# Optimization experiments

Measured on AMD Instinct MI355X. Metric: run time of the kernel, lower is better.

The kernel has to match this reference:

```python
import jax, jax.numpy as jnp
import numpy as np

B, N, EMB, H, DH = 1, 196, 256, 8, 32
HID = 4 * EMB
EPS = 1e-5
SCALE = 16.0  # emb_size ** 0.5 (torch code scales by emb_size, not head_dim)


def _ln(x, w, b):
    m = jnp.mean(x, axis=-1, keepdims=True)
    v = jnp.mean((x - m) ** 2, axis=-1, keepdims=True)
    return (x - m) * jax.lax.rsqrt(v + EPS) * w + b


def _qkv(x, W, bias):
    # rearrange 'b n (h d qkv) -> qkv b h n d'
    t = (x @ W + bias).reshape(B, N, H, DH, 3)
    t = jnp.transpose(t, (4, 0, 2, 1, 3))
    return t[0], t[1], t[2]


def _attn(q, k, v, Wp, bp):
    att = jax.nn.softmax(jnp.einsum('bhqd,bhkd->bhqk', q, k) / SCALE, axis=-1)
    o = jnp.einsum('bhqk,bhkd->bhqd', att, v)
    o = jnp.transpose(o, (0, 2, 1, 3)).reshape(B, N, EMB)  # b n (h d)
    return o @ Wp + bp


def _ff(x, W1, b1, W2, b2):
    return jax.nn.gelu(x @ W1 + b1, approximate=False) @ W2 + b2


def _recon(x):
    x = x.reshape(B, 14, 14, 16, 16)
    x = jnp.transpose(x, (0, 3, 4, 1, 2))
    return x.reshape(B, 1, 224, 224)


def setup_inputs() -> dict:
    key = jax.random.key(0)
    ks = jax.random.split(key, 16)
    rn = lambda k, shape: jax.random.normal(k, shape, jnp.float32) * 0.02
    d = {
        'vis_emb': jax.random.normal(ks[0], (B, N, EMB), jnp.float32),
        'ir_emb': jax.random.normal(ks[1], (B, N, EMB), jnp.float32),
        'ln1v_w': jnp.ones((EMB,), jnp.float32), 'ln1v_b': jnp.zeros((EMB,), jnp.float32),
        'ln1i_w': jnp.ones((EMB,), jnp.float32), 'ln1i_b': jnp.zeros((EMB,), jnp.float32),
        'ln2v_w': jnp.ones((EMB,), jnp.float32), 'ln2v_b': jnp.zeros((EMB,), jnp.float32),
        'ln2i_w': jnp.ones((EMB,), jnp.float32), 'ln2i_b': jnp.zeros((EMB,), jnp.float32),
        'Wqkv_v': rn(ks[2], (EMB, 3 * EMB)), 'bqkv_v': jnp.zeros((3 * EMB,), jnp.float32),
        'Wqkv_i': rn(ks[3], (EMB, 3 * EMB)), 'bqkv_i': jnp.zeros((3 * EMB,), jnp.float32),
        'Wp_v': rn(ks[4], (EMB, EMB)), 'bp_v': jnp.zeros((EMB,), jnp.float32),
        'Wp_i': rn(ks[5], (EMB, EMB)), 'bp_i': jnp.zeros((EMB,), jnp.float32),
        'W1v': rn(ks[6], (EMB, HID)), 'b1v': jnp.zeros((HID,), jnp.float32),
        'W2v': rn(ks[7], (HID, EMB)), 'b2v': jnp.zeros((EMB,), jnp.float32),
        'W1i': rn(ks[8], (EMB, HID)), 'b1i': jnp.zeros((HID,), jnp.float32),
        'W2i': rn(ks[9], (HID, EMB)), 'b2i': jnp.zeros((EMB,), jnp.float32),
    }
    return d


def reference(vis_emb, ir_emb, ln1v_w, ln1v_b, ln1i_w, ln1i_b, ln2v_w, ln2v_b,
              ln2i_w, ln2i_b, Wqkv_v, bqkv_v, Wqkv_i, bqkv_i, Wp_v, bp_v,
              Wp_i, bp_i, W1v, b1v, W2v, b2v, W1i, b1i, W2i, b2i):
    nv = _ln(vis_emb, ln1v_w, ln1v_b)
    ni = _ln(ir_emb, ln1i_w, ln1i_b)
    qv, kv_, vv = _qkv(vis_emb, Wqkv_v, bqkv_v)
    qi, ki, vi = _qkv(ir_emb, Wqkv_i, bqkv_i)
    cross_v2i = _attn(qv, ki, vi, Wp_v, bp_v)   # vis queries attend ir k/v
    cross_i2v = _attn(qi, kv_, vv, Wp_i, bp_i)  # ir queries attend vis k/v
    rv = nv + cross_v2i
    ri = ni + cross_i2v
    lv = _ln(rv, ln2v_w, ln2v_b)
    li = _ln(ri, ln2i_w, ln2i_b)
    ov = _ff(lv, W1v, b1v, W2v, b2v) + lv
    oi = _ff(li, W1i, b1i, W2i, b2i) + li
    return jnp.concatenate([_recon(oi), _recon(ov)], axis=1)  # (1,2,224,224)
```

## Files before the change

kernel.cpp:

```cpp
#include <hip/hip_runtime.h>
#include <math.h>

#define NT   196
#define EMB  256
#define NH   8
#define DH   32
#define HID  1024
#define EPSV 1e-5f


__global__ __launch_bounds__(256) void k1_qkv(
    const float* __restrict__ vis, const float* __restrict__ ir,
    const float* __restrict__ Wqkv_v, const float* __restrict__ bqkv_v,
    const float* __restrict__ Wqkv_i, const float* __restrict__ bqkv_i,
    float* __restrict__ Q, float* __restrict__ Kq, float* __restrict__ Vq)
{
    const int b = blockIdx.x;
    const int s = b / 147;
    const int rem = b % 147;
    const int mt = rem / 3;
    const int cg = rem % 3;
    const int n0 = mt * 4;
    const int t = threadIdx.x;

    const float* x    = (s == 0) ? vis    : ir;
    const float* W    = (s == 0) ? Wqkv_v : Wqkv_i;
    const float* bias = (s == 0) ? bqkv_v : bqkv_i;

    __shared__ float xsT[EMB * 4];
    __shared__ float pp[4 * 4 * 256];

    {
        int r = t >> 6, c4 = (t & 63) * 4;
        float4 xv = *(const float4*)&x[(n0 + r) * EMB + c4];
        xsT[(c4 + 0) * 4 + r] = xv.x;
        xsT[(c4 + 1) * 4 + r] = xv.y;
        xsT[(c4 + 2) * 4 + r] = xv.z;
        xsT[(c4 + 3) * 4 + r] = xv.w;
    }
    __syncthreads();

    const int cq = t & 63, ks = t >> 6;
    const int col0 = cg * 256 + cq * 4;
    const float* Wb = W + col0;
    float4 a0 = {0,0,0,0}, a1 = a0, a2 = a0, a3 = a0;
    #pragma unroll 8
    for (int kk = ks * 64; kk < ks * 64 + 64; kk++) {
        float4 w4 = *(const float4*)&Wb[kk * 768];
        float4 xr = *(const float4*)&xsT[kk * 4];
        a0.x = fmaf(xr.x, w4.x, a0.x); a0.y = fmaf(xr.x, w4.y, a0.y);
        a0.z = fmaf(xr.x, w4.z, a0.z); a0.w = fmaf(xr.x, w4.w, a0.w);
        a1.x = fmaf(xr.y, w4.x, a1.x); a1.y = fmaf(xr.y, w4.y, a1.y);
        a1.z = fmaf(xr.y, w4.z, a1.z); a1.w = fmaf(xr.y, w4.w, a1.w);
        a2.x = fmaf(xr.z, w4.x, a2.x); a2.y = fmaf(xr.z, w4.y, a2.y);
        a2.z = fmaf(xr.z, w4.z, a2.z); a2.w = fmaf(xr.z, w4.w, a2.w);
        a3.x = fmaf(xr.w, w4.x, a3.x); a3.y = fmaf(xr.w, w4.y, a3.y);
        a3.z = fmaf(xr.w, w4.z, a3.z); a3.w = fmaf(xr.w, w4.w, a3.w);
    }
    *(float4*)&pp[(ks * 4 + 0) * 256 + cq * 4] = a0;
    *(float4*)&pp[(ks * 4 + 1) * 256 + cq * 4] = a1;
    *(float4*)&pp[(ks * 4 + 2) * 256 + cq * 4] = a2;
    *(float4*)&pp[(ks * 4 + 3) * 256 + cq * 4] = a3;
    __syncthreads();

    const int col = cg * 256 + t;
    const int h = col / 96, rr = col % 96, d = rr / 3, q = rr % 3;
    float* dst = (q == 0) ? Q : (q == 1 ? Kq : Vq);
    const float bval = bias[col];
    #pragma unroll
    for (int r = 0; r < 4; r++) {
        float v = pp[(0 * 4 + r) * 256 + t] + pp[(1 * 4 + r) * 256 + t]
                + pp[(2 * 4 + r) * 256 + t] + pp[(3 * 4 + r) * 256 + t] + bval;
        dst[((s * NH + h) * NT + n0 + r) * DH + d] = v;
    }
}

__global__ __launch_bounds__(256) void k2_attn(
    const float* __restrict__ Q, const float* __restrict__ Kq,
    const float* __restrict__ Vq, float* __restrict__ AO)
{
    const int b  = blockIdx.x;
    const int s  = b / 112;
    const int rm = b % 112;
    const int h  = rm / 14;
    const int rt = rm % 14;
    const int t    = threadIdx.x;
    const int wv   = t >> 6;
    const int lane = t & 63;

    __shared__ float kl[NT * 33];
    __shared__ float vl[NT * 33];
    __shared__ float pb[4][NT];

    const float4* Ks4 = (const float4*)(Kq + ((1 - s) * NH + h) * NT * DH);
    const float4* Vs4 = (const float4*)(Vq + ((1 - s) * NH + h) * NT * DH);
    for (int idx = t; idx < NT * 8; idx += 256) {
        int j = idx >> 3, d4 = (idx & 7) * 4;
        float4 kv = Ks4[idx];
        kl[j * 33 + d4 + 0] = kv.x; kl[j * 33 + d4 + 1] = kv.y;
        kl[j * 33 + d4 + 2] = kv.z; kl[j * 33 + d4 + 3] = kv.w;
        float4 vv = Vs4[idx];
        vl[j * 33 + d4 + 0] = vv.x; vl[j * 33 + d4 + 1] = vv.y;
        vl[j * 33 + d4 + 2] = vv.z; vl[j * 33 + d4 + 3] = vv.w;
    }
    __syncthreads();

    const float* Qs = Q + ((s * NH + h) * NT) * DH;
    const bool v3 = (lane + 192) < NT;
    const int  j3 = v3 ? (lane + 192) : 0;

    for (int it = 0; it < 4; it++) {
        int lr = it * 4 + wv;
        bool act = lr < 14;
        int i = rt * 14 + lr;
        float inv_sum = 0.0f;
        if (act) {
            float qreg[DH];
            #pragma unroll
            for (int d = 0; d < DH; d++) qreg[d] = Qs[i * DH + d];
            float s0 = 0.f, s1 = 0.f, s2 = 0.f, s3 = 0.f;
            #pragma unroll
            for (int d = 0; d < DH; d++) {
                float qd = qreg[d];
                s0 = fmaf(qd, kl[(lane      ) * 33 + d], s0);
                s1 = fmaf(qd, kl[(lane +  64) * 33 + d], s1);
                s2 = fmaf(qd, kl[(lane + 128) * 33 + d], s2);
                s3 = fmaf(qd, kl[ j3          * 33 + d], s3);
            }
            const float sc = 1.0f / 16.0f;
            s0 *= sc; s1 *= sc; s2 *= sc; s3 *= sc;
            float m = fmaxf(fmaxf(s0, s1), v3 ? fmaxf(s2, s3) : s2);
            #pragma unroll
            for (int mk = 32; mk >= 1; mk >>= 1) m = fmaxf(m, __shfl_xor(m, mk));
            float p0 = expf(s0 - m), p1 = expf(s1 - m), p2 = expf(s2 - m);
            float p3 = v3 ? expf(s3 - m) : 0.0f;
            float ls = p0 + p1 + p2 + p3;
            #pragma unroll
            for (int mk = 32; mk >= 1; mk >>= 1) ls += __shfl_xor(ls, mk);
            inv_sum = 1.0f / ls;
            pb[wv][lane]       = p0;
            pb[wv][lane +  64] = p1;
            pb[wv][lane + 128] = p2;
            if (v3) pb[wv][lane + 192] = p3;
        }
        __syncthreads();
        if (act) {
            int d = lane & 31, half = lane >> 5;
            float o = 0.0f;
            int jb = half * 98;
            for (int jj = 0; jj < 98; jj++) {
                int j = jb + jj;
                o = fmaf(pb[wv][j], vl[j * 33 + d], o);
            }
            o += __shfl_xor(o, 32);
            if (lane < 32) AO[(s * NT + i) * EMB + h * DH + d] = o * inv_sum;
        }
        __syncthreads();
    }
}

__global__ __launch_bounds__(256) void k3_proj_ln2(
    const float* __restrict__ vis, const float* __restrict__ ir,
    const float* __restrict__ AO,
    const float* __restrict__ ln1v_w, const float* __restrict__ ln1v_b,
    const float* __restrict__ ln1i_w, const float* __restrict__ ln1i_b,
    const float* __restrict__ Wp_v, const float* __restrict__ bp_v,
    const float* __restrict__ Wp_i, const float* __restrict__ bp_i,
    const float* __restrict__ ln2v_w, const float* __restrict__ ln2v_b,
    const float* __restrict__ ln2i_w, const float* __restrict__ ln2i_b,
    float* __restrict__ LV)
{
    const int b = blockIdx.x;
    const int s = b / 49;
    const int n0 = (b % 49) * 4;
    const int t = threadIdx.x;

    const float* x   = (s == 0) ? vis    : ir;
    const float* W   = (s == 0) ? Wp_v   : Wp_i;
    const float* bp  = (s == 0) ? bp_v   : bp_i;
    const float* l1w = (s == 0) ? ln1v_w : ln1i_w;
    const float* l1b = (s == 0) ? ln1v_b : ln1i_b;
    const float* l2w = (s == 0) ? ln2v_w : ln2i_w;
    const float* l2b = (s == 0) ? ln2v_b : ln2i_b;

    __shared__ float aoT[EMB * 4];
    __shared__ float pp[4 * 4 * 256];
    __shared__ float nvb[4 * 256];
    __shared__ float rbuf[4 * 256];

    const int r = t >> 6, lane = t & 63, c4 = lane * 4;

    {
        float4 xv = *(const float4*)&x[(n0 + r) * EMB + c4];
        float sum = xv.x + xv.y + xv.z + xv.w;
        float sq  = xv.x*xv.x + xv.y*xv.y + xv.z*xv.z + xv.w*xv.w;
        #pragma unroll
        for (int mk = 32; mk >= 1; mk >>= 1) {
            sum += __shfl_xor(sum, mk);
            sq  += __shfl_xor(sq,  mk);
        }
        float mean = sum * (1.0f / EMB);
        float inv  = rsqrtf(sq * (1.0f / EMB) - mean * mean + EPSV);
        float4 wv4 = *(const float4*)&l1w[c4];
        float4 bv4 = *(const float4*)&l1b[c4];
        nvb[r * 256 + c4 + 0] = (xv.x - mean) * inv * wv4.x + bv4.x;
        nvb[r * 256 + c4 + 1] = (xv.y - mean) * inv * wv4.y + bv4.y;
        nvb[r * 256 + c4 + 2] = (xv.z - mean) * inv * wv4.z + bv4.z;
        nvb[r * 256 + c4 + 3] = (xv.w - mean) * inv * wv4.w + bv4.w;
        float4 av = *(const float4*)&AO[(s * NT + n0 + r) * EMB + c4];
        aoT[(c4 + 0) * 4 + r] = av.x;
        aoT[(c4 + 1) * 4 + r] = av.y;
        aoT[(c4 + 2) * 4 + r] = av.z;
        aoT[(c4 + 3) * 4 + r] = av.w;
    }
    __syncthreads();

    const int cq = t & 63, ks = t >> 6;
    const int col0 = cq * 4;
    const float* Wb = W + col0;
    float4 a0 = {0,0,0,0}, a1 = a0, a2 = a0, a3 = a0;
    #pragma unroll 8
    for (int kk = ks * 64; kk < ks * 64 + 64; kk++) {
        float4 w4 = *(const float4*)&Wb[kk * EMB];
        float4 xr = *(const float4*)&aoT[kk * 4];
        a0.x = fmaf(xr.x, w4.x, a0.x); a0.y = fmaf(xr.x, w4.y, a0.y);
        a0.z = fmaf(xr.x, w4.z, a0.z); a0.w = fmaf(xr.x, w4.w, a0.w);
        a1.x = fmaf(xr.y, w4.x, a1.x); a1.y = fmaf(xr.y, w4.y, a1.y);
        a1.z = fmaf(xr.y, w4.z, a1.z); a1.w = fmaf(xr.y, w4.w, a1.w);
        a2.x = fmaf(xr.z, w4.x, a2.x); a2.y = fmaf(xr.z, w4.y, a2.y);
        a2.z = fmaf(xr.z, w4.z, a2.z); a2.w = fmaf(xr.z, w4.w, a2.w);
        a3.x = fmaf(xr.w, w4.x, a3.x); a3.y = fmaf(xr.w, w4.y, a3.y);
        a3.z = fmaf(xr.w, w4.z, a3.z); a3.w = fmaf(xr.w, w4.w, a3.w);
    }
    *(float4*)&pp[(ks * 4 + 0) * 256 + cq * 4] = a0;
    *(float4*)&pp[(ks * 4 + 1) * 256 + cq * 4] = a1;
    *(float4*)&pp[(ks * 4 + 2) * 256 + cq * 4] = a2;
    *(float4*)&pp[(ks * 4 + 3) * 256 + cq * 4] = a3;
    __syncthreads();

    {
        const float bval = bp[t];
        #pragma unroll
        for (int r2 = 0; r2 < 4; r2++) {
            float v = pp[(0 * 4 + r2) * 256 + t] + pp[(1 * 4 + r2) * 256 + t]
                    + pp[(2 * 4 + r2) * 256 + t] + pp[(3 * 4 + r2) * 256 + t]
                    + bval + nvb[r2 * 256 + t];
            rbuf[r2 * 256 + t] = v;
        }
    }
    __syncthreads();

    {
        float4 rv = *(const float4*)&rbuf[r * 256 + c4];
        float sum = rv.x + rv.y + rv.z + rv.w;
        float sq  = rv.x*rv.x + rv.y*rv.y + rv.z*rv.z + rv.w*rv.w;
        #pragma unroll
        for (int mk = 32; mk >= 1; mk >>= 1) {
            sum += __shfl_xor(sum, mk);
            sq  += __shfl_xor(sq,  mk);
        }
        float mean = sum * (1.0f / EMB);
        float inv  = rsqrtf(sq * (1.0f / EMB) - mean * mean + EPSV);
        float4 wv4 = *(const float4*)&l2w[c4];
        float4 bv4 = *(const float4*)&l2b[c4];
        float4 o;
        o.x = (rv.x - mean) * inv * wv4.x + bv4.x;
        o.y = (rv.y - mean) * inv * wv4.y + bv4.y;
        o.z = (rv.z - mean) * inv * wv4.z + bv4.z;
        o.w = (rv.w - mean) * inv * wv4.w + bv4.w;
        *(float4*)&LV[(s * NT + n0 + r) * EMB + c4] = o;
    }
}

__global__ __launch_bounds__(256) void k4_ffn1(
    const float* __restrict__ LV,
    const float* __restrict__ W1v, const float* __restrict__ b1v,
    const float* __restrict__ W1i, const float* __restrict__ b1i,
    float* __restrict__ HH)
{
    const int b = blockIdx.x;
    const int s = b / 196;
    const int rem = b % 196;
    const int mt = rem / 4;
    const int cg = rem % 4;
    const int n0 = mt * 4;
    const int t = threadIdx.x;

    const float* W  = (s == 0) ? W1v : W1i;
    const float* bb = (s == 0) ? b1v : b1i;

    __shared__ float xsT[EMB * 4];
    __shared__ float pp[4 * 4 * 256];

    {
        int r = t >> 6, c4 = (t & 63) * 4;
        float4 xv = *(const float4*)&LV[(s * NT + n0 + r) * EMB + c4];
        xsT[(c4 + 0) * 4 + r] = xv.x;
        xsT[(c4 + 1) * 4 + r] = xv.y;
        xsT[(c4 + 2) * 4 + r] = xv.z;
        xsT[(c4 + 3) * 4 + r] = xv.w;
    }
    __syncthreads();

    const int cq = t & 63, ks = t >> 6;
    const int col0 = cg * 256 + cq * 4;
    const float* Wb = W + col0;
    float4 a0 = {0,0,0,0}, a1 = a0, a2 = a0, a3 = a0;
    #pragma unroll 8
    for (int kk = ks * 64; kk < ks * 64 + 64; kk++) {
        float4 w4 = *(const float4*)&Wb[kk * HID];
        float4 xr = *(const float4*)&xsT[kk * 4];
        a0.x = fmaf(xr.x, w4.x, a0.x); a0.y = fmaf(xr.x, w4.y, a0.y);
        a0.z = fmaf(xr.x, w4.z, a0.z); a0.w = fmaf(xr.x, w4.w, a0.w);
        a1.x = fmaf(xr.y, w4.x, a1.x); a1.y = fmaf(xr.y, w4.y, a1.y);
        a1.z = fmaf(xr.y, w4.z, a1.z); a1.w = fmaf(xr.y, w4.w, a1.w);
        a2.x = fmaf(xr.z, w4.x, a2.x); a2.y = fmaf(xr.z, w4.y, a2.y);
        a2.z = fmaf(xr.z, w4.z, a2.z); a2.w = fmaf(xr.z, w4.w, a2.w);
        a3.x = fmaf(xr.w, w4.x, a3.x); a3.y = fmaf(xr.w, w4.y, a3.y);
        a3.z = fmaf(xr.w, w4.z, a3.z); a3.w = fmaf(xr.w, w4.w, a3.w);
    }
    *(float4*)&pp[(ks * 4 + 0) * 256 + cq * 4] = a0;
    *(float4*)&pp[(ks * 4 + 1) * 256 + cq * 4] = a1;
    *(float4*)&pp[(ks * 4 + 2) * 256 + cq * 4] = a2;
    *(float4*)&pp[(ks * 4 + 3) * 256 + cq * 4] = a3;
    __syncthreads();

    const int col = cg * 256 + t;
    const float bval = bb[col];
    #pragma unroll
    for (int r = 0; r < 4; r++) {
        float v = pp[(0 * 4 + r) * 256 + t] + pp[(1 * 4 + r) * 256 + t]
                + pp[(2 * 4 + r) * 256 + t] + pp[(3 * 4 + r) * 256 + t] + bval;
        float g = 0.5f * v * (1.0f + erff(v * 0.7071067811865475f));
        HH[(s * NT + n0 + r) * HID + col] = g;
    }
}

__global__ __launch_bounds__(256) void k5_ffn2_out(
    const float* __restrict__ HH, const float* __restrict__ LV,
    const float* __restrict__ W2v, const float* __restrict__ b2v,
    const float* __restrict__ W2i, const float* __restrict__ b2i,
    float* __restrict__ out)
{
    const int b = blockIdx.x;
    const int s = b / 49;
    const int n0 = (b % 49) * 4;
    const int t = threadIdx.x;

    const float* W  = (s == 0) ? W2v : W2i;
    const float* bb = (s == 0) ? b2v : b2i;

    __shared__ float hhT[HID * 4];
    __shared__ float pp[4 * 4 * 256];

    {
        int r = t >> 6, lane = t & 63;
        #pragma unroll
        for (int rd = 0; rd < 4; rd++) {
            int c4 = rd * 256 + lane * 4;
            float4 hv = *(const float4*)&HH[(s * NT + n0 + r) * HID + c4];
            hhT[(c4 + 0) * 4 + r] = hv.x;
            hhT[(c4 + 1) * 4 + r] = hv.y;
            hhT[(c4 + 2) * 4 + r] = hv.z;
            hhT[(c4 + 3) * 4 + r] = hv.w;
        }
    }
    __syncthreads();

    const int cq = t & 63, ks = t >> 6;
    const int col0 = cq * 4;
    const float* Wb = W + col0;
    float4 a0 = {0,0,0,0}, a1 = a0, a2 = a0, a3 = a0;
    #pragma unroll 8
    for (int kk = ks * 256; kk < ks * 256 + 256; kk++) {
        float4 w4 = *(const float4*)&Wb[kk * EMB];
        float4 xr = *(const float4*)&hhT[kk * 4];
        a0.x = fmaf(xr.x, w4.x, a0.x); a0.y = fmaf(xr.x, w4.y, a0.y);
        a0.z = fmaf(xr.x, w4.z, a0.z); a0.w = fmaf(xr.x, w4.w, a0.w);
        a1.x = fmaf(xr.y, w4.x, a1.x); a1.y = fmaf(xr.y, w4.y, a1.y);
        a1.z = fmaf(xr.y, w4.z, a1.z); a1.w = fmaf(xr.y, w4.w, a1.w);
        a2.x = fmaf(xr.z, w4.x, a2.x); a2.y = fmaf(xr.z, w4.y, a2.y);
        a2.z = fmaf(xr.z, w4.z, a2.z); a2.w = fmaf(xr.z, w4.w, a2.w);
        a3.x = fmaf(xr.w, w4.x, a3.x); a3.y = fmaf(xr.w, w4.y, a3.y);
        a3.z = fmaf(xr.w, w4.z, a3.z); a3.w = fmaf(xr.w, w4.w, a3.w);
    }
    *(float4*)&pp[(ks * 4 + 0) * 256 + cq * 4] = a0;
    *(float4*)&pp[(ks * 4 + 1) * 256 + cq * 4] = a1;
    *(float4*)&pp[(ks * 4 + 2) * 256 + cq * 4] = a2;
    *(float4*)&pp[(ks * 4 + 3) * 256 + cq * 4] = a3;
    __syncthreads();

    const float bval = bb[t];
    const int p1 = t >> 4, p2 = t & 15;
    const int ch = (s == 0) ? 1 : 0;
    #pragma unroll
    for (int r = 0; r < 4; r++) {
        int n = n0 + r;
        float v = pp[(0 * 4 + r) * 256 + t] + pp[(1 * 4 + r) * 256 + t]
                + pp[(2 * 4 + r) * 256 + t] + pp[(3 * 4 + r) * 256 + t]
                + bval + LV[(s * NT + n) * EMB + t];
        int n1 = n / 14, n2 = n % 14;
        int f = p1 * 3136 + p2 * 196 + n1 * 14 + n2;
        out[ch * 50176 + f] = v;
    }
}

extern "C" void kernel_launch(void* const* d_in, const int* in_sizes, int n_in,
                              void* d_out, int out_size, void* d_ws, size_t ws_size,
                              hipStream_t stream)
{
    const float* vis    = (const float*)d_in[0];
    const float* ir     = (const float*)d_in[1];
    const float* ln1v_w = (const float*)d_in[2];
    const float* ln1v_b = (const float*)d_in[3];
    const float* ln1i_w = (const float*)d_in[4];
    const float* ln1i_b = (const float*)d_in[5];
    const float* ln2v_w = (const float*)d_in[6];
    const float* ln2v_b = (const float*)d_in[7];
    const float* ln2i_w = (const float*)d_in[8];
    const float* ln2i_b = (const float*)d_in[9];
    const float* Wqkv_v = (const float*)d_in[10];
    const float* bqkv_v = (const float*)d_in[11];
    const float* Wqkv_i = (const float*)d_in[12];
    const float* bqkv_i = (const float*)d_in[13];
    const float* Wp_v   = (const float*)d_in[14];
    const float* bp_v   = (const float*)d_in[15];
    const float* Wp_i   = (const float*)d_in[16];
    const float* bp_i   = (const float*)d_in[17];
    const float* W1v    = (const float*)d_in[18];
    const float* b1v    = (const float*)d_in[19];
    const float* W2v    = (const float*)d_in[20];
    const float* b2v    = (const float*)d_in[21];
    const float* W1i    = (const float*)d_in[22];
    const float* b1i    = (const float*)d_in[23];
    const float* W2i    = (const float*)d_in[24];
    const float* b2i    = (const float*)d_in[25];

    float* ws = (float*)d_ws;
    float* Q  = ws;
    float* K  = ws + 100352;
    float* V  = ws + 200704;
    float* AO = ws + 301056;
    float* LV = ws + 401408;
    float* HH = ws + 501760;

    k1_qkv<<<294, 256, 0, stream>>>(vis, ir, Wqkv_v, bqkv_v, Wqkv_i, bqkv_i, Q, K, V);
    k2_attn<<<224, 256, 0, stream>>>(Q, K, V, AO);
    k3_proj_ln2<<<98, 256, 0, stream>>>(vis, ir, AO, ln1v_w, ln1v_b, ln1i_w, ln1i_b,
                                        Wp_v, bp_v, Wp_i, bp_i,
                                        ln2v_w, ln2v_b, ln2i_w, ln2i_b, LV);
    k4_ffn1<<<392, 256, 0, stream>>>(LV, W1v, b1v, W1i, b1i, HH);
    k5_ffn2_out<<<98, 256, 0, stream>>>(HH, LV, W2v, b2v, W2i, b2i, (float*)d_out);
}
```

Before: 170.0 us.

## Fuse projection, LN2, FFN1 GELU, and FFN2 into one tail kernel

Merges the former k3 (proj+LN2), k4 (FFN1+GELU), and k5 (FFN2+output) into a single kernel per 4-token tile, keeping the LN2 output and GELU hidden activations in shared memory. This removes two kernel launches and the global-memory round trips for LV and HH. The cost is that FFN1 now runs on only 98 blocks instead of 392, each thread computing a full 256-deep K loop. Larger shared memory (about 52KB) also lowers occupancy. A GEMM macro factors out the repeated panel loop.

```diff
diff --git a/kernel.cpp b/kernel.cpp
--- a/kernel.cpp
+++ b/kernel.cpp
@@ -8,6 +8,28 @@
 #define HID  1024
 #define EPSV 1e-5f
 
+#define GEMM_PANEL(Wptr, ldw, xsT, pp, cq, ks, KITER)                          \
+    {                                                                          \
+        const float* Wb = (Wptr);                                              \
+        float4 a0 = {0,0,0,0}, a1 = a0, a2 = a0, a3 = a0;                      \
+        _Pragma("unroll 8")                                                    \
+        for (int kk = (ks) * (KITER); kk < (ks) * (KITER) + (KITER); kk++) {   \
+            float4 w4 = *(const float4*)&Wb[kk * (ldw)];                       \
+            float4 xr = *(const float4*)&(xsT)[kk * 4];                        \
+            a0.x = fmaf(xr.x, w4.x, a0.x); a0.y = fmaf(xr.x, w4.y, a0.y);      \
+            a0.z = fmaf(xr.x, w4.z, a0.z); a0.w = fmaf(xr.x, w4.w, a0.w);      \
+            a1.x = fmaf(xr.y, w4.x, a1.x); a1.y = fmaf(xr.y, w4.y, a1.y);      \
+            a1.z = fmaf(xr.y, w4.z, a1.z); a1.w = fmaf(xr.y, w4.w, a1.w);      \
+            a2.x = fmaf(xr.z, w4.x, a2.x); a2.y = fmaf(xr.z, w4.y, a2.y);      \
+            a2.z = fmaf(xr.z, w4.z, a2.z); a2.w = fmaf(xr.z, w4.w, a2.w);      \
+            a3.x = fmaf(xr.w, w4.x, a3.x); a3.y = fmaf(xr.w, w4.y, a3.y);      \
+            a3.z = fmaf(xr.w, w4.z, a3.z); a3.w = fmaf(xr.w, w4.w, a3.w);      \
+        }                                                                      \
+        *(float4*)&(pp)[((ks) * 4 + 0) * 256 + (cq) * 4] = a0;                 \
+        *(float4*)&(pp)[((ks) * 4 + 1) * 256 + (cq) * 4] = a1;                 \
+        *(float4*)&(pp)[((ks) * 4 + 2) * 256 + (cq) * 4] = a2;                 \
+        *(float4*)&(pp)[((ks) * 4 + 3) * 256 + (cq) * 4] = a3;                 \
+    }
 
 __global__ __launch_bounds__(256) void k1_qkv(
     const float* __restrict__ vis, const float* __restrict__ ir,
@@ -18,9 +40,8 @@
     const int b = blockIdx.x;
     const int s = b / 147;
     const int rem = b % 147;
-    const int mt = rem / 3;
+    const int n0 = (rem / 3) * 4;
     const int cg = rem % 3;
-    const int n0 = mt * 4;
     const int t = threadIdx.x;
 
     const float* x    = (s == 0) ? vis    : ir;
@@ -41,26 +62,7 @@
     __syncthreads();
 
     const int cq = t & 63, ks = t >> 6;
-    const int col0 = cg * 256 + cq * 4;
-    const float* Wb = W + col0;
-    float4 a0 = {0,0,0,0}, a1 = a0, a2 = a0, a3 = a0;
-    #pragma unroll 8
-    for (int kk = ks * 64; kk < ks * 64 + 64; kk++) {
-        float4 w4 = *(const float4*)&Wb[kk * 768];
-        float4 xr = *(const float4*)&xsT[kk * 4];
-        a0.x = fmaf(xr.x, w4.x, a0.x); a0.y = fmaf(xr.x, w4.y, a0.y);
-        a0.z = fmaf(xr.x, w4.z, a0.z); a0.w = fmaf(xr.x, w4.w, a0.w);
-        a1.x = fmaf(xr.y, w4.x, a1.x); a1.y = fmaf(xr.y, w4.y, a1.y);
-        a1.z = fmaf(xr.y, w4.z, a1.z); a1.w = fmaf(xr.y, w4.w, a1.w);
-        a2.x = fmaf(xr.z, w4.x, a2.x); a2.y = fmaf(xr.z, w4.y, a2.y);
-        a2.z = fmaf(xr.z, w4.z, a2.z); a2.w = fmaf(xr.z, w4.w, a2.w);
-        a3.x = fmaf(xr.w, w4.x, a3.x); a3.y = fmaf(xr.w, w4.y, a3.y);
-        a3.z = fmaf(xr.w, w4.z, a3.z); a3.w = fmaf(xr.w, w4.w, a3.w);
-    }
-    *(float4*)&pp[(ks * 4 + 0) * 256 + cq * 4] = a0;
-    *(float4*)&pp[(ks * 4 + 1) * 256 + cq * 4] = a1;
-    *(float4*)&pp[(ks * 4 + 2) * 256 + cq * 4] = a2;
-    *(float4*)&pp[(ks * 4 + 3) * 256 + cq * 4] = a3;
+    GEMM_PANEL(W + cg * 256 + cq * 4, 768, xsT, pp, cq, ks, 64);
     __syncthreads();
 
     const int col = cg * 256 + t;
@@ -159,7 +161,7 @@
     }
 }
 
-__global__ __launch_bounds__(256) void k3_proj_ln2(
+__global__ __launch_bounds__(256) void k3_tail(
     const float* __restrict__ vis, const float* __restrict__ ir,
     const float* __restrict__ AO,
     const float* __restrict__ ln1v_w, const float* __restrict__ ln1v_b,
@@ -168,7 +170,11 @@
     const float* __restrict__ Wp_i, const float* __restrict__ bp_i,
     const float* __restrict__ ln2v_w, const float* __restrict__ ln2v_b,
     const float* __restrict__ ln2i_w, const float* __restrict__ ln2i_b,
-    float* __restrict__ LV)
+    const float* __restrict__ W1v, const float* __restrict__ b1v,
+    const float* __restrict__ W1i, const float* __restrict__ b1i,
+    const float* __restrict__ W2v, const float* __restrict__ b2v,
+    const float* __restrict__ W2i, const float* __restrict__ b2i,
+    float* __restrict__ out)
 {
     const int b = blockIdx.x;
     const int s = b / 49;
@@ -176,19 +182,28 @@
     const int t = threadIdx.x;
 
     const float* x   = (s == 0) ? vis    : ir;
-    const float* W   = (s == 0) ? Wp_v   : Wp_i;
+    const float* Wp  = (s == 0) ? Wp_v   : Wp_i;
     const float* bp  = (s == 0) ? bp_v   : bp_i;
     const float* l1w = (s == 0) ? ln1v_w : ln1i_w;
     const float* l1b = (s == 0) ? ln1v_b : ln1i_b;
     const float* l2w = (s == 0) ? ln2v_w : ln2i_w;
     const float* l2b = (s == 0) ? ln2v_b : ln2i_b;
-
-    __shared__ float aoT[EMB * 4];
-    __shared__ float pp[4 * 4 * 256];
-    __shared__ float nvb[4 * 256];
-    __shared__ float rbuf[4 * 256];
+    const float* W1  = (s == 0) ? W1v    : W1i;
+    const float* bb1 = (s == 0) ? b1v    : b1i;
+    const float* W2  = (s == 0) ? W2v    : W2i;
+    const float* bb2 = (s == 0) ? b2v    : b2i;
+
+    __shared__ float smem[13312];
+    float* aoT  = smem;
+    float* nvb  = smem + 1024;
+    float* rbuf = smem + 2048;
+    float* lvb  = smem + 3072;
+    float* lvT  = smem + 4096;
+    float* hhT  = smem + 5120;
+    float* pp   = smem + 9216;
 
     const int r = t >> 6, lane = t & 63, c4 = lane * 4;
+    const int cq = t & 63, ks = t >> 6;
 
     {
         float4 xv = *(const float4*)&x[(n0 + r) * EMB + c4];
@@ -215,27 +230,7 @@
     }
     __syncthreads();
 
-    const int cq = t & 63, ks = t >> 6;
-    const int col0 = cq * 4;
-    const float* Wb = W + col0;
-    float4 a0 = {0,0,0,0}, a1 = a0, a2 = a0, a3 = a0;
-    #pragma unroll 8
-    for (int kk = ks * 64; kk < ks * 64 + 64; kk++) {
-        float4 w4 = *(const float4*)&Wb[kk * EMB];
-        float4 xr = *(const float4*)&aoT[kk * 4];
-        a0.x = fmaf(xr.x, w4.x, a0.x); a0.y = fmaf(xr.x, w4.y, a0.y);
-        a0.z = fmaf(xr.x, w4.z, a0.z); a0.w = fmaf(xr.x, w4.w, a0.w);
-        a1.x = fmaf(xr.y, w4.x, a1.x); a1.y = fmaf(xr.y, w4.y, a1.y);
-        a1.z = fmaf(xr.y, w4.z, a1.z); a1.w = fmaf(xr.y, w4.w, a1.w);
-        a2.x = fmaf(xr.z, w4.x, a2.x); a2.y = fmaf(xr.z, w4.y, a2.y);
-        a2.z = fmaf(xr.z, w4.z, a2.z); a2.w = fmaf(xr.z, w4.w, a2.w);
-        a3.x = fmaf(xr.w, w4.x, a3.x); a3.y = fmaf(xr.w, w4.y, a3.y);
-        a3.z = fmaf(xr.w, w4.z, a3.z); a3.w = fmaf(xr.w, w4.w, a3.w);
-    }
-    *(float4*)&pp[(ks * 4 + 0) * 256 + cq * 4] = a0;
-    *(float4*)&pp[(ks * 4 + 1) * 256 + cq * 4] = a1;
-    *(float4*)&pp[(ks * 4 + 2) * 256 + cq * 4] = a2;
-    *(float4*)&pp[(ks * 4 + 3) * 256 + cq * 4] = a3;
+    GEMM_PANEL(Wp + cq * 4, EMB, aoT, pp, cq, ks, 64);
     __syncthreads();
 
     {
@@ -249,7 +244,6 @@
         }
     }
     __syncthreads();
-
     {
         float4 rv = *(const float4*)&rbuf[r * 256 + c4];
         float sum = rv.x + rv.y + rv.z + rv.w;
@@ -268,140 +262,65 @@
         o.y = (rv.y - mean) * inv * wv4.y + bv4.y;
         o.z = (rv.z - mean) * inv * wv4.z + bv4.z;
         o.w = (rv.w - mean) * inv * wv4.w + bv4.w;
-        *(float4*)&LV[(s * NT + n0 + r) * EMB + c4] = o;
-    }
-}
-
-__global__ __launch_bounds__(256) void k4_ffn1(
-    const float* __restrict__ LV,
-    const float* __restrict__ W1v, const float* __restrict__ b1v,
-    const float* __restrict__ W1i, const float* __restrict__ b1i,
-    float* __restrict__ HH)
-{
-    const int b = blockIdx.x;
-    const int s = b / 196;
-    const int rem = b % 196;
-    const int mt = rem / 4;
-    const int cg = rem % 4;
-    const int n0 = mt * 4;
-    const int t = threadIdx.x;
-
-    const float* W  = (s == 0) ? W1v : W1i;
-    const float* bb = (s == 0) ? b1v : b1i;
-
-    __shared__ float xsT[EMB * 4];
-    __shared__ float pp[4 * 4 * 256];
-
-    {
-        int r = t >> 6, c4 = (t & 63) * 4;
-        float4 xv = *(const float4*)&LV[(s * NT + n0 + r) * EMB + c4];
-        xsT[(c4 + 0) * 4 + r] = xv.x;
-        xsT[(c4 + 1) * 4 + r] = xv.y;
-        xsT[(c4 + 2) * 4 + r] = xv.z;
-        xsT[(c4 + 3) * 4 + r] = xv.w;
-    }
-    __syncthreads();
-
-    const int cq = t & 63, ks = t >> 6;
-    const int col0 = cg * 256 + cq * 4;
-    const float* Wb = W + col0;
-    float4 a0 = {0,0,0,0}, a1 = a0, a2 = a0, a3 = a0;
-    #pragma unroll 8
-    for (int kk = ks * 64; kk < ks * 64 + 64; kk++) {
-        float4 w4 = *(const float4*)&Wb[kk * HID];
-        float4 xr = *(const float4*)&xsT[kk * 4];
-        a0.x = fmaf(xr.x, w4.x, a0.x); a0.y = fmaf(xr.x, w4.y, a0.y);
-        a0.z = fmaf(xr.x, w4.z, a0.z); a0.w = fmaf(xr.x, w4.w, a0.w);
-        a1.x = fmaf(xr.y, w4.x, a1.x); a1.y = fmaf(xr.y, w4.y, a1.y);
-        a1.z = fmaf(xr.y, w4.z, a1.z); a1.w = fmaf(xr.y, w4.w, a1.w);
-        a2.x = fmaf(xr.z, w4.x, a2.x); a2.y = fmaf(xr.z, w4.y, a2.y);
-        a2.z = fmaf(xr.z, w4.z, a2.z); a2.w = fmaf(xr.z, w4.w, a2.w);
-        a3.x = fmaf(xr.w, w4.x, a3.x); a3.y = fmaf(xr.w, w4.y, a3.y);
-        a3.z = fmaf(xr.w, w4.z, a3.z); a3.w = fmaf(xr.w, w4.w, a3.w);
-    }
-    *(float4*)&pp[(ks * 4 + 0) * 256 + cq * 4] = a0;
-    *(float4*)&pp[(ks * 4 + 1) * 256 + cq * 4] = a1;
-    *(float4*)&pp[(ks * 4 + 2) * 256 + cq * 4] = a2;
-    *(float4*)&pp[(ks * 4 + 3) * 256 + cq * 4] = a3;
-    __syncthreads();
-
-    const int col = cg * 256 + t;
-    const float bval = bb[col];
-    #pragma unroll
-    for (int r = 0; r < 4; r++) {
-        float v = pp[(0 * 4 + r) * 256 + t] + pp[(1 * 4 + r) * 256 + t]
-                + pp[(2 * 4 + r) * 256 + t] + pp[(3 * 4 + r) * 256 + t] + bval;
-        float g = 0.5f * v * (1.0f + erff(v * 0.7071067811865475f));
-        HH[(s * NT + n0 + r) * HID + col] = g;
-    }
-}
-
-__global__ __launch_bounds__(256) void k5_ffn2_out(
-    const float* __restrict__ HH, const float* __restrict__ LV,
-    const float* __restrict__ W2v, const float* __restrict__ b2v,
-    const float* __restrict__ W2i, const float* __restrict__ b2i,
-    float* __restrict__ out)
-{
-    const int b = blockIdx.x;
-    const int s = b / 49;
-    const int n0 = (b % 49) * 4;
-    const int t = threadIdx.x;
-
-    const float* W  = (s == 0) ? W2v : W2i;
-    const float* bb = (s == 0) ? b2v : b2i;
-
-    __shared__ float hhT[HID * 4];
-    __shared__ float pp[4 * 4 * 256];
-
-    {
-        int r = t >> 6, lane = t & 63;
+        *(float4*)&lvb[r * 256 + c4] = o;
+        lvT[(c4 + 0) * 4 + r] = o.x;
+        lvT[(c4 + 1) * 4 + r] = o.y;
+        lvT[(c4 + 2) * 4 + r] = o.z;
+        lvT[(c4 + 3) * 4 + r] = o.w;
+    }
+    __syncthreads();
+
+    {
+        const int cD = t * 4;
+        float4 a0 = {0,0,0,0}, a1 = a0, a2 = a0, a3 = a0;
+        #pragma unroll 8
+        for (int kk = 0; kk < EMB; kk++) {
+            float4 w4 = *(const float4*)&W1[kk * HID + cD];
+            float4 xr = *(const float4*)&lvT[kk * 4];
+            a0.x = fmaf(xr.x, w4.x, a0.x); a0.y = fmaf(xr.x, w4.y, a0.y);
+            a0.z = fmaf(xr.x, w4.z, a0.z); a0.w = fmaf(xr.x, w4.w, a0.w);
+            a1.x = fmaf(xr.y, w4.x, a1.x); a1.y = fmaf(xr.y, w4.y, a1.y);
+            a1.z = fmaf(xr.y, w4.z, a1.z); a1.w = fmaf(xr.y, w4.w, a1.w);
+            a2.x = fmaf(xr.z, w4.x, a2.x); a2.y = fmaf(xr.z, w4.y, a2.y);
+            a2.z = fmaf(xr.z, w4.z, a2.z); a2.w = fmaf(xr.z, w4.w, a2.w);
+            a3.x = fmaf(xr.w, w4.x, a3.x); a3.y = fmaf(xr.w, w4.y, a3.y);
+            a3.z = fmaf(xr.w, w4.z, a3.z); a3.w = fmaf(xr.w, w4.w, a3.w);
+        }
+        float4 bv4 = *(const float4*)&bb1[cD];
+        a0.x += bv4.x; a0.y += bv4.y; a0.z += bv4.z; a0.w += bv4.w;
+        a1.x += bv4.x; a1.y += bv4.y; a1.z += bv4.z; a1.w += bv4.w;
+        a2.x += bv4.x; a2.y += bv4.y; a2.z += bv4.z; a2.w += bv4.w;
+        a3.x += bv4.x; a3.y += bv4.y; a3.z += bv4.z; a3.w += bv4.w;
+        const float k = 0.7071067811865475f;
+        #define GELU(v) (0.5f * (v) * (1.0f + erff((v) * k)))
+        float4 h0 = { GELU(a0.x), GELU(a1.x), GELU(a2.x), GELU(a3.x) };
+        float4 h1 = { GELU(a0.y), GELU(a1.y), GELU(a2.y), GELU(a3.y) };
+        float4 h2 = { GELU(a0.z), GELU(a1.z), GELU(a2.z), GELU(a3.z) };
+        float4 h3 = { GELU(a0.w), GELU(a1.w), GELU(a2.w), GELU(a3.w) };
+        #undef GELU
+        *(float4*)&hhT[(cD + 0) * 4] = h0;
+        *(float4*)&hhT[(cD + 1) * 4] = h1;
+        *(float4*)&hhT[(cD + 2) * 4] = h2;
+        *(float4*)&hhT[(cD + 3) * 4] = h3;
+    }
+    __syncthreads();
+
+    GEMM_PANEL(W2 + cq * 4, EMB, hhT, pp, cq, ks, 256);
+    __syncthreads();
+    {
+        const float bval = bb2[t];
+        const int p1 = t >> 4, p2 = t & 15;
+        const int ch = (s == 0) ? 1 : 0;
         #pragma unroll
-        for (int rd = 0; rd < 4; rd++) {
-            int c4 = rd * 256 + lane * 4;
-            float4 hv = *(const float4*)&HH[(s * NT + n0 + r) * HID + c4];
-            hhT[(c4 + 0) * 4 + r] = hv.x;
-            hhT[(c4 + 1) * 4 + r] = hv.y;
-            hhT[(c4 + 2) * 4 + r] = hv.z;
-            hhT[(c4 + 3) * 4 + r] = hv.w;
-        }
-    }
-    __syncthreads();
-
-    const int cq = t & 63, ks = t >> 6;
-    const int col0 = cq * 4;
-    const float* Wb = W + col0;
-    float4 a0 = {0,0,0,0}, a1 = a0, a2 = a0, a3 = a0;
-    #pragma unroll 8
-    for (int kk = ks * 256; kk < ks * 256 + 256; kk++) {
-        float4 w4 = *(const float4*)&Wb[kk * EMB];
-        float4 xr = *(const float4*)&hhT[kk * 4];
-        a0.x = fmaf(xr.x, w4.x, a0.x); a0.y = fmaf(xr.x, w4.y, a0.y);
-        a0.z = fmaf(xr.x, w4.z, a0.z); a0.w = fmaf(xr.x, w4.w, a0.w);
-        a1.x = fmaf(xr.y, w4.x, a1.x); a1.y = fmaf(xr.y, w4.y, a1.y);
-        a1.z = fmaf(xr.y, w4.z, a1.z); a1.w = fmaf(xr.y, w4.w, a1.w);
-        a2.x = fmaf(xr.z, w4.x, a2.x); a2.y = fmaf(xr.z, w4.y, a2.y);
-        a2.z = fmaf(xr.z, w4.z, a2.z); a2.w = fmaf(xr.z, w4.w, a2.w);
-        a3.x = fmaf(xr.w, w4.x, a3.x); a3.y = fmaf(xr.w, w4.y, a3.y);
-        a3.z = fmaf(xr.w, w4.z, a3.z); a3.w = fmaf(xr.w, w4.w, a3.w);
-    }
-    *(float4*)&pp[(ks * 4 + 0) * 256 + cq * 4] = a0;
-    *(float4*)&pp[(ks * 4 + 1) * 256 + cq * 4] = a1;
-    *(float4*)&pp[(ks * 4 + 2) * 256 + cq * 4] = a2;
-    *(float4*)&pp[(ks * 4 + 3) * 256 + cq * 4] = a3;
-    __syncthreads();
-
-    const float bval = bb[t];
-    const int p1 = t >> 4, p2 = t & 15;
-    const int ch = (s == 0) ? 1 : 0;
-    #pragma unroll
-    for (int r = 0; r < 4; r++) {
-        int n = n0 + r;
-        float v = pp[(0 * 4 + r) * 256 + t] + pp[(1 * 4 + r) * 256 + t]
-                + pp[(2 * 4 + r) * 256 + t] + pp[(3 * 4 + r) * 256 + t]
-                + bval + LV[(s * NT + n) * EMB + t];
-        int n1 = n / 14, n2 = n % 14;
-        int f = p1 * 3136 + p2 * 196 + n1 * 14 + n2;
-        out[ch * 50176 + f] = v;
+        for (int r2 = 0; r2 < 4; r2++) {
+            int n = n0 + r2;
+            float v = pp[(0 * 4 + r2) * 256 + t] + pp[(1 * 4 + r2) * 256 + t]
+                    + pp[(2 * 4 + r2) * 256 + t] + pp[(3 * 4 + r2) * 256 + t]
+                    + bval + lvb[r2 * 256 + t];
+            int n1 = n / 14, n2 = n % 14;
+            int f = p1 * 3136 + p2 * 196 + n1 * 14 + n2;
+            out[ch * 50176 + f] = v;
+        }
     }
 }
 
@@ -441,14 +360,14 @@
     float* K  = ws + 100352;
     float* V  = ws + 200704;
     float* AO = ws + 301056;
-    float* LV = ws + 401408;
-    float* HH = ws + 501760;
 
     k1_qkv<<<294, 256, 0, stream>>>(vis, ir, Wqkv_v, bqkv_v, Wqkv_i, bqkv_i, Q, K, V);
     k2_attn<<<224, 256, 0, stream>>>(Q, K, V, AO);
-    k3_proj_ln2<<<98, 256, 0, stream>>>(vis, ir, AO, ln1v_w, ln1v_b, ln1i_w, ln1i_b,
-                                        Wp_v, bp_v, Wp_i, bp_i,
-                                        ln2v_w, ln2v_b, ln2i_w, ln2i_b, LV);
-    k4_ffn1<<<392, 256, 0, stream>>>(LV, W1v, b1v, W1i, b1i, HH);
-    k5_ffn2_out<<<98, 256, 0, stream>>>(HH, LV, W2v, b2v, W2i, b2i, (float*)d_out);
+    k3_tail<<<98, 256, 0, stream>>>(vis, ir, AO,
+                                    ln1v_w, ln1v_b, ln1i_w, ln1i_b,
+                                    Wp_v, bp_v, Wp_i, bp_i,
+                                    ln2v_w, ln2v_b, ln2i_w, ln2i_b,
+                                    W1v, b1v, W1i, b1i,
+                                    W2v, b2v, W2i, b2i,
+                                    (float*)d_out);
 }
```

Result: faster. 162.0 us (-4.7%).
